# Kernel tuning notes

Measured on AMD Instinct MI355X. Metric: run time of the kernel, lower is better.

## Reference

```python
import jax, jax.numpy as jnp
import numpy as np

N = 65536   # nodes
D = 128     # in_dim == emb_dim (required by GRUCell usage)
E = 524288  # edges, pre-sorted by topological level
L = 8       # number of topological levels (edge_masks)


def _gru(x, h, Wi, Wh, bi, bh):
    # torch.nn.GRUCell semantics
    gi = x @ Wi.T + bi            # [*, 3D]
    gh = h @ Wh.T + bh
    ir, iz, i_n = jnp.split(gi, 3, axis=-1)
    hr, hz, h_n = jnp.split(gh, 3, axis=-1)
    r = jax.nn.sigmoid(ir + hr)
    z = jax.nn.sigmoid(iz + hz)
    n = jnp.tanh(i_n + r * h_n)
    return (1.0 - z) * n + z * h


def _direction(h_prev, j_lev, i_lev, ea_lev, We, be, Wa, ba, Wi, Wh, bi, bh):
    # j = message source (h_j gathered), i = aggregation target (segment index)
    n_nodes = h_prev.shape[0]
    # roots = nodes never appearing as aggregation target -> GRU with zero hidden
    root = ~jnp.zeros((n_nodes,), bool).at[i_lev.reshape(-1)].set(True)
    h = jnp.where(root[:, None], _gru(h_prev, jnp.zeros_like(h_prev), Wi, Wh, bi, bh), 0.0)

    def step(h, lev):
        j, i, ea = lev                       # [El], [El], [El, D]
        e = ea @ We.T + be                   # edge_lin
        q = h_prev[i]                        # h_prev_i
        k = h[j] + e                         # h_j + edge_emb
        v = h[j]
        alpha = (jnp.concatenate([q, k], axis=-1) @ Wa.T + ba)[:, 0]  # [El]
        # segment softmax over aggregation index i (numerically stable)
        m = jax.lax.stop_gradient(jax.ops.segment_max(alpha, i, num_segments=n_nodes))
        ex = jnp.exp(alpha - m[i])
        den = jax.ops.segment_sum(ex, i, num_segments=n_nodes)
        a = ex / den[i]
        msg = jax.ops.segment_sum(a[:, None] * v, i, num_segments=n_nodes)  # [N, D]
        mask = jnp.zeros((n_nodes,), bool).at[i].set(True)
        h_new = _gru(h_prev, msg, Wi, Wh, bi, bh)
        return jnp.where(mask[:, None], h_new, h), None

    h, _ = jax.lax.scan(step, h, (j_lev, i_lev, ea_lev))
    return h


def setup_inputs() -> dict:
    key = jax.random.key(0)
    ks = jax.random.split(key, 24)
    p = lambda k, shape: (0.05 * jax.random.normal(k, shape)).astype(jnp.float32)
    inp = {
        'x': jax.random.normal(ks[0], (N, D), jnp.float32),
        'edge_index': jax.random.randint(ks[1], (2, E), 0, N, dtype=jnp.int32),
        'edge_attr': jax.random.normal(ks[2], (E, D), jnp.float32),
        'num_levels': L,
        # forward-direction AttnConv + GRUCell params
        'We_f': p(ks[3], (D, D)), 'be_f': p(ks[4], (D,)),
        'Wa_f': p(ks[5], (1, 2 * D)), 'ba_f': p(ks[6], (1,)),
        'Wi_f': p(ks[7], (3 * D, D)), 'Wh_f': p(ks[8], (3 * D, D)),
        'bi_f': p(ks[9], (3 * D,)), 'bh_f': p(ks[10], (3 * D,)),
        # backward-direction params
        'We_b': p(ks[11], (D, D)), 'be_b': p(ks[12], (D,)),
        'Wa_b': p(ks[13], (1, 2 * D)), 'ba_b': p(ks[14], (1,)),
        'Wi_b': p(ks[15], (3 * D, D)), 'Wh_b': p(ks[16], (3 * D, D)),
        'bi_b': p(ks[17], (3 * D,)), 'bh_b': p(ks[18], (3 * D,)),
    }
    return inp


def reference(x, edge_index, edge_attr, num_levels,
              We_f, be_f, Wa_f, ba_f, Wi_f, Wh_f, bi_f, bh_f,
              We_b, be_b, Wa_b, ba_b, Wi_b, Wh_b, bi_b, bh_b):
    El = edge_index.shape[1] // num_levels
    src = edge_index[0].reshape(num_levels, El)
    dst = edge_index[1].reshape(num_levels, El)
    ea = edge_attr.reshape(num_levels, El, -1)
    # forward pass over levels: flow source->target, aggregate at dst
    h_fwd = _direction(x, src, dst, ea, We_f, be_f, Wa_f, ba_f, Wi_f, Wh_f, bi_f, bh_f)
    # fnb: backward pass takes h_fwd as h_prev; flow target->source (aggregate at src),
    # levels iterated in reverse
    h_bwd = _direction(h_fwd, dst[::-1], src[::-1], ea[::-1],
                       We_b, be_b, Wa_b, ba_b, Wi_b, Wh_b, bi_b, bh_b)
    return jax.nn.relu(h_bwd)
```

## Files before the change

kernel.cpp:

```cpp
#include <hip/hip_runtime.h>
#include <cstdint>
#include <cstddef>

constexpr int N_NODES = 65536;
constexpr int D       = 128;
constexpr int E_EDGES = 524288;
constexpr int LVLS    = 8;
constexpr int EL      = E_EDGES / LVLS;
constexpr int OSTR    = 65540;

typedef unsigned int  u32;
typedef unsigned short u16;
typedef __attribute__((ext_vector_type(8)))  short short8;
typedef __attribute__((ext_vector_type(16))) float f32x16;

__device__ __forceinline__ float sigmoidf_(float x) { return 1.0f / (1.0f + expf(-x)); }

__device__ __forceinline__ u32 bf_hi(float f) {
    u32 x = __float_as_uint(f);
    return (x + 0x7fffu + ((x >> 16) & 1u)) >> 16;
}
__device__ __forceinline__ float bf_f(u32 hbits) { return __uint_as_float(hbits << 16); }

__device__ __forceinline__ int swz(int row, int kbyte) {
    return row * 64 + (kbyte ^ ((row & 3) << 4));
}

__device__ __forceinline__ void gload_lds16(const void* g, void* l) {
    __builtin_amdgcn_global_load_lds(
        (const __attribute__((address_space(1))) unsigned int*)g,
        (__attribute__((address_space(3))) unsigned int*)l, 16, 0, 0);
}

__device__ __forceinline__ float wave_sum(float v) {
#pragma unroll
    for (int off = 32; off > 0; off >>= 1) v += __shfl_down(v, off, 64);
    return v;
}

__global__ __launch_bounds__(256)
void prep_kernel(const float* __restrict__ We_f, const float* __restrict__ Wa_f,
                 const float* __restrict__ be_f, const float* __restrict__ ba_f,
                 const float* __restrict__ We_b, const float* __restrict__ Wa_b,
                 const float* __restrict__ be_b, const float* __restrict__ ba_b,
                 float* __restrict__ u_f, float* __restrict__ u_b, float* __restrict__ cst)
{
    int t = threadIdx.x;
    if (t < 128) {
        float s = 0.f;
        for (int d = 0; d < 128; ++d) s = fmaf(We_f[d * 128 + t], Wa_f[128 + d], s);
        u_f[t] = s;
    } else {
        int c = t - 128;
        float s = 0.f;
        for (int d = 0; d < 128; ++d) s = fmaf(We_b[d * 128 + c], Wa_b[128 + d], s);
        u_b[c] = s;
    }
    if (t == 0) {
        float s = 0.f;
        for (int d = 0; d < 128; ++d) s = fmaf(be_f[d], Wa_f[128 + d], s);
        cst[0] = s + ba_f[0];
    }
    if (t == 255) {
        float s = 0.f;
        for (int d = 0; d < 128; ++d) s = fmaf(be_b[d], Wa_b[128 + d], s);
        cst[1] = s + ba_b[0];
    }
}

__global__ __launch_bounds__(256)
void convert_w(const float* __restrict__ W0, const float* __restrict__ W1,
               const float* __restrict__ W2, const float* __restrict__ W3,
               u16* __restrict__ hi4, u16* __restrict__ lo4)
{
    const float* Ws[4] = {W0, W1, W2, W3};
    int m = blockIdx.y;
    int i = blockIdx.x * 256 + threadIdx.x;
    int rw = i >> 7, k = i & 127;
    float v = Ws[m][i];
    u32 hb = bf_hi(v);
    hi4[(size_t)m * 49152 + i] = (u16)hb;
    if (rw >= 256)
        lo4[(size_t)m * 16384 + (size_t)(rw - 256) * 128 + k] = (u16)bf_hi(v - bf_f(hb));
}

__global__ __launch_bounds__(256)
void convert_x(const float* __restrict__ x, unsigned char* __restrict__ xhi,
               unsigned char* __restrict__ xlo)
{
    int idx = blockIdx.x * 256 + threadIdx.x;
    int n = idx >> 6, d = (idx & 63) << 1;
    float2 v = *reinterpret_cast<const float2*>(x + (size_t)n * 128 + d);
    u32 h0 = bf_hi(v.x), h1 = bf_hi(v.y);
    u32 l0 = bf_hi(v.x - bf_f(h0)), l1 = bf_hi(v.y - bf_f(h1));
    size_t off = (size_t)n * 256 + (size_t)d * 2;
    *reinterpret_cast<u32*>(xhi + off) = h0 | (h1 << 16);
    *reinterpret_cast<u32*>(xlo + off) = l0 | (l1 << 16);
}

__global__ __launch_bounds__(256)
void edot_kernel(const float* __restrict__ ea, const float* __restrict__ u_f,
                 const float* __restrict__ u_b, const float* __restrict__ cst,
                 float* __restrict__ edot_f, float* __restrict__ edot_b)
{
    int wv = threadIdx.x >> 6, lane = threadIdx.x & 63;
    int e = blockIdx.x * 4 + wv;
    if (e >= E_EDGES) return;
    int d = lane << 1;
    float2 v  = *reinterpret_cast<const float2*>(ea + (size_t)e * 128 + d);
    float2 uf = *reinterpret_cast<const float2*>(u_f + d);
    float2 ub = *reinterpret_cast<const float2*>(u_b + d);
    float af = wave_sum(v.x * uf.x + v.y * uf.y);
    float ab = wave_sum(v.x * ub.x + v.y * ub.y);
    if (lane == 0) {
        edot_f[e] = af + cst[0];
        edot_b[e] = ab + cst[1];
    }
}

__global__ __launch_bounds__(256)
void count_flags(const int* __restrict__ ei, int* __restrict__ counts,
                 int* __restrict__ flag_f, int* __restrict__ flag_b)
{
    int e = blockIdx.x * 256 + threadIdx.x;
    int lv = e >> 16;
    int s = ei[e], t = ei[E_EDGES + e];
    atomicAdd(&counts[(size_t)lv * 65536 + t], 1);
    atomicAdd(&counts[(size_t)(8 + lv) * 65536 + s], 1);
    flag_f[t] = 1;
    flag_b[s] = 1;
}

__global__ __launch_bounds__(1024)
void scan_compact(const int* __restrict__ counts, int* __restrict__ offs,
                  int* __restrict__ rows, int* __restrict__ cnts)
{
    __shared__ int sbuf[1024];
    __shared__ int nbuf[1024];
    int dl = blockIdx.x;
    const int4* c4 = reinterpret_cast<const int4*>(counts + (size_t)dl * 65536);
    int* o = offs + (size_t)dl * OSTR;
    int* rw = rows + (size_t)dl * 65536;
    int t = threadIdx.x;
    int cv[64];
#pragma unroll 4
    for (int k4 = 0; k4 < 16; ++k4) {
        int4 v = c4[t * 16 + k4];
        cv[k4 * 4 + 0] = v.x; cv[k4 * 4 + 1] = v.y;
        cv[k4 * 4 + 2] = v.z; cv[k4 * 4 + 3] = v.w;
    }
    int s = 0, nz = 0;
#pragma unroll
    for (int k = 0; k < 64; ++k) { s += cv[k]; nz += (cv[k] > 0); }
    sbuf[t] = s;
    nbuf[t] = nz;
    __syncthreads();
    int val = s, nval = nz;
    for (int off = 1; off < 1024; off <<= 1) {
        int add  = (t >= off) ? sbuf[t - off] : 0;
        int nadd = (t >= off) ? nbuf[t - off] : 0;
        __syncthreads();
        val += add;
        nval += nadd;
        sbuf[t] = val;
        nbuf[t] = nval;
        __syncthreads();
    }
    int run  = val - s;
    int nrun = nval - nz;
    int base = t * 64;
    int4* o4 = reinterpret_cast<int4*>(o + base);
#pragma unroll 4
    for (int k4 = 0; k4 < 16; ++k4) {
        int4 ov;
        ov.x = run; run += cv[k4 * 4 + 0];
        ov.y = run; run += cv[k4 * 4 + 1];
        ov.z = run; run += cv[k4 * 4 + 2];
        ov.w = run; run += cv[k4 * 4 + 3];
        o4[k4] = ov;
#pragma unroll
        for (int q = 0; q < 4; ++q)
            if (cv[k4 * 4 + q] > 0) rw[nrun++] = base + k4 * 4 + q;
    }
    if (t == 1023) { o[65536] = val; cnts[dl] = nval; }
}

__global__ __launch_bounds__(256)
void fill_csr(const int* __restrict__ ei, const float* __restrict__ edot_f,
              const float* __restrict__ edot_b, const int* __restrict__ offs,
              int* __restrict__ cursor, int2* __restrict__ csr)
{
    int idx = blockIdx.x * 256 + threadIdx.x;
    int dir = idx >= E_EDGES;
    int ge = dir ? idx - E_EDGES : idx;
    int lv = ge >> 16;
    int dl = dir * 8 + lv;
    int i = dir ? ei[ge] : ei[E_EDGES + ge];
    int j = dir ? ei[E_EDGES + ge] : ei[ge];
    int pos = offs[(size_t)dl * OSTR + i] + atomicAdd(&cursor[(size_t)dl * 65536 + i], 1);
    int2 v;
    v.x = j;
    v.y = __float_as_int(dir ? edot_b[ge] : edot_f[ge]);
    csr[(size_t)dl * EL + pos] = v;
}

__global__ __launch_bounds__(256)
void root_init(const float* __restrict__ hp, const int* __restrict__ flag,
               const float* __restrict__ Wi, const float* __restrict__ bi,
               const float* __restrict__ bh, const float* __restrict__ wa,
               float* __restrict__ h, unsigned char* __restrict__ h_hi,
               unsigned char* __restrict__ h_lo,
               float* __restrict__ qdot, float* __restrict__ hdot)
{
    int wv = threadIdx.x >> 6, lane = threadIdx.x & 63;
    int n = blockIdx.x * 4 + wv;
    int d = lane << 1;
    const float* hprow = hp + (size_t)n * 128;
    float2 hpv = *reinterpret_cast<const float2*>(hprow + d);
    float qd = wave_sum(hpv.x * wa[d] + hpv.y * wa[d + 1]);
    if (lane == 0) qdot[n] = qd;
    bool root = (flag[n] == 0);
    float hv[2] = {0.f, 0.f};
    if (root) {
#pragma unroll
        for (int q = 0; q < 2; ++q) {
            int dd = d + q;
            float g0 = bi[dd], g1 = bi[dd + 128], g2 = bi[dd + 256];
            for (int k = 0; k < 128; ++k) {
                float a = hprow[k];
                g0 = fmaf(a, Wi[(size_t)dd * 128 + k], g0);
                g1 = fmaf(a, Wi[(size_t)(dd + 128) * 128 + k], g1);
                g2 = fmaf(a, Wi[(size_t)(dd + 256) * 128 + k], g2);
            }
            float rr = sigmoidf_(g0 + bh[dd]);
            float zz = sigmoidf_(g1 + bh[dd + 128]);
            float nn = tanhf(g2 + rr * bh[dd + 256]);
            hv[q] = (1.f - zz) * nn;
        }
        *reinterpret_cast<float2*>(h + (size_t)n * 128 + d) = make_float2(hv[0], hv[1]);
        u32 hb0 = bf_hi(hv[0]), hb1 = bf_hi(hv[1]);
        u32 lb0 = bf_hi(hv[0] - bf_f(hb0)), lb1 = bf_hi(hv[1] - bf_f(hb1));
        size_t off = (size_t)n * 256 + (size_t)d * 2;
        *reinterpret_cast<u32*>(h_hi + off) = hb0 | (hb1 << 16);
        *reinterpret_cast<u32*>(h_lo + off) = lb0 | (lb1 << 16);
    }
    float hd = wave_sum(hv[0] * wa[128 + d] + hv[1] * wa[128 + d + 1]);
    if (lane == 0) hdot[n] = root ? hd : 0.f;
}

__global__ __launch_bounds__(256)
void attn_msg(const int* __restrict__ pcnt, const int* __restrict__ rows,
              const int* __restrict__ offs, const int2* __restrict__ csr,
              const float* __restrict__ qdot, const float* __restrict__ hdot,
              const float* __restrict__ h, unsigned char* __restrict__ msg_hi,
              unsigned char* __restrict__ msg_lo)
{
    int cnt = *pcnt;
    int l31 = threadIdx.x & 31;
    int hid = (blockIdx.x * 256 + threadIdx.x) >> 5;
    int nh = (gridDim.x * 256) >> 5;
    int d4 = l31 << 2;
    for (int r = hid; r < cnt; r += nh) {
        int i = rows[r];
        int o0 = offs[i], o1 = offs[i + 1];
        float qi = qdot[i];
        float den = 0.f;
        float4 acc = make_float4(0.f, 0.f, 0.f, 0.f);
        for (int e = o0; e < o1; ++e) {
            int2 je = csr[e];
            float ex = expf(qi + hdot[je.x] + __int_as_float(je.y));
            float4 hv = *reinterpret_cast<const float4*>(h + (size_t)je.x * 128 + d4);
            den += ex;
            acc.x = fmaf(ex, hv.x, acc.x);
            acc.y = fmaf(ex, hv.y, acc.y);
            acc.z = fmaf(ex, hv.z, acc.z);
            acc.w = fmaf(ex, hv.w, acc.w);
        }
        float inv = 1.f / den;
        float m0 = acc.x * inv, m1 = acc.y * inv, m2 = acc.z * inv, m3 = acc.w * inv;
        u32 h0 = bf_hi(m0), h1 = bf_hi(m1), h2 = bf_hi(m2), h3 = bf_hi(m3);
        u32 l0 = bf_hi(m0 - bf_f(h0)), l1 = bf_hi(m1 - bf_f(h1));
        u32 l2 = bf_hi(m2 - bf_f(h2)), l3 = bf_hi(m3 - bf_f(h3));
        size_t off = (size_t)r * 256 + (size_t)d4 * 2;
        *reinterpret_cast<uint2*>(msg_hi + off) = make_uint2(h0 | (h1 << 16), h2 | (h3 << 16));
        *reinterpret_cast<uint2*>(msg_lo + off) = make_uint2(l0 | (l1 << 16), l2 | (l3 << 16));
    }
}

__global__ __launch_bounds__(512, 1)
void gemm_gru(const unsigned char* __restrict__ msg_hi, const unsigned char* __restrict__ msg_lo,
              const unsigned char* __restrict__ hp_hi, const unsigned char* __restrict__ hp_lo,
              const u16* __restrict__ Whhi, const u16* __restrict__ Whlo,
              const u16* __restrict__ Wihi, const u16* __restrict__ Wilo,
              const int* __restrict__ pcnt, const int* __restrict__ rows,
              const float* __restrict__ bi, const float* __restrict__ bh,
              const float* __restrict__ wa,
              float* __restrict__ h, unsigned char* __restrict__ h_hi,
              unsigned char* __restrict__ h_lo, float* __restrict__ hdot)
{
    __shared__ __align__(16) unsigned char smem[32768 + 65536 + 2048 + 512];
    unsigned char* As = smem;
    unsigned char* Bs = smem + 32768;
    float* red   = (float*)(smem + 98304);
    int* rowsLds = (int*)(smem + 98304 + 2048);

    const int tid = threadIdx.x;
    const int cnt = *pcnt;
    const int row0 = blockIdx.x * 128;
    if (row0 >= cnt) return;

    if (tid < 128) {
        int gr = row0 + tid;
        rowsLds[tid] = (gr < cnt) ? rows[gr] : 0;
    }
    __syncthreads();

    const int lane = tid & 63, wv = tid >> 6;
    const int q = wv & 3, mh = wv >> 2;
    const int l31 = lane & 31, l5 = lane >> 5;

    const int rwA = wv * 16 + (lane >> 2);
    const int slA = ((lane & 3) << 4) ^ ((rwA & 3) << 4);
    const size_t baseA0 = (size_t)(row0 + rwA) * 256 + slA;
    const size_t baseA1 = (size_t)rowsLds[rwA] * 256 + slA;
    size_t bsrc[3];
#pragma unroll
    for (int k = 0; k < 3; ++k) {
        int rwB = wv * 48 + k * 16 + (lane >> 2);
        bsrc[k] = (size_t)rwB * 256 + (((lane & 3) << 4) ^ ((rwB & 3) << 4));
    }
    const int rwL = wv * 16 + (lane >> 2);
    const size_t lsrc = (size_t)rwL * 256 + (((lane & 3) << 4) ^ ((rwL & 3) << 4));

    f32x16 acc[2][3];
#pragma unroll
    for (int mt = 0; mt < 2; ++mt)
#pragma unroll
        for (int g = 0; g < 3; ++g) acc[mt][g] = (f32x16)0.0f;
    f32x16 ghn[2];

    auto STAGE = [&](int t, int b) {
        int ph = t >> 2, ks = t & 3;
        size_t ko = (size_t)ks * 64;
        const unsigned char* Ahi = ph ? hp_hi : msg_hi;
        const unsigned char* Alo = ph ? hp_lo : msg_lo;
        size_t ab = (ph ? baseA1 : baseA0) + ko;
        unsigned char* Ad = As + b * 16384 + wv * 1024;
        gload_lds16(Ahi + ab, Ad);
        gload_lds16(Alo + ab, Ad + 8192);
        const unsigned char* Bh = (const unsigned char*)(ph ? Wihi : Whhi);
        const unsigned char* Bl = (const unsigned char*)(ph ? Wilo : Whlo);
        unsigned char* Bd = Bs + b * 32768;
#pragma unroll
        for (int k = 0; k < 3; ++k)
            gload_lds16(Bh + bsrc[k] + ko, Bd + (wv * 3 + k) * 1024);
        gload_lds16(Bl + lsrc + ko, Bd + 24576 + wv * 1024);
    };

    STAGE(0, 0);
    for (int t = 0; t < 8; ++t) {
        int b = t & 1;
        if (t < 7) STAGE(t + 1, b ^ 1);
        __builtin_amdgcn_sched_barrier(0);
        if (t < 7) asm volatile("s_waitcnt vmcnt(6)");
        else       asm volatile("s_waitcnt vmcnt(0)");
        __builtin_amdgcn_s_barrier();
        __builtin_amdgcn_sched_barrier(0);

        const unsigned char* Ab = As + b * 16384;
        const unsigned char* Bb = Bs + b * 32768;
#pragma unroll
        for (int kh = 0; kh < 2; ++kh) {
            short8 a[2][2];
#pragma unroll
            for (int mt = 0; mt < 2; ++mt)
#pragma unroll
                for (int hf = 0; hf < 2; ++hf)
                    a[mt][hf] = *reinterpret_cast<const short8*>(
                        Ab + hf * 8192 + swz(mh * 64 + mt * 32 + l31, kh * 32 + l5 * 16));
            short8 b0 = *reinterpret_cast<const short8*>(
                Bb + swz(q * 32 + l31, kh * 32 + l5 * 16));
            short8 b1 = *reinterpret_cast<const short8*>(
                Bb + swz(q * 32 + 128 + l31, kh * 32 + l5 * 16));
            short8 b2 = *reinterpret_cast<const short8*>(
                Bb + swz(q * 32 + 256 + l31, kh * 32 + l5 * 16));
            short8 bl2 = *reinterpret_cast<const short8*>(
                Bb + 24576 + swz(q * 32 + l31, kh * 32 + l5 * 16));
#pragma unroll
            for (int mt = 0; mt < 2; ++mt) {
                acc[mt][0] = __builtin_amdgcn_mfma_f32_32x32x16_bf16(a[mt][0], b0, acc[mt][0], 0, 0, 0);
                acc[mt][0] = __builtin_amdgcn_mfma_f32_32x32x16_bf16(a[mt][1], b0, acc[mt][0], 0, 0, 0);
                acc[mt][1] = __builtin_amdgcn_mfma_f32_32x32x16_bf16(a[mt][0], b1, acc[mt][1], 0, 0, 0);
                acc[mt][1] = __builtin_amdgcn_mfma_f32_32x32x16_bf16(a[mt][1], b1, acc[mt][1], 0, 0, 0);
                acc[mt][2] = __builtin_amdgcn_mfma_f32_32x32x16_bf16(a[mt][0], b2, acc[mt][2], 0, 0, 0);
                acc[mt][2] = __builtin_amdgcn_mfma_f32_32x32x16_bf16(a[mt][0], bl2, acc[mt][2], 0, 0, 0);
                acc[mt][2] = __builtin_amdgcn_mfma_f32_32x32x16_bf16(a[mt][1], b2, acc[mt][2], 0, 0, 0);
            }
        }
        if (t == 3) {
            ghn[0] = acc[0][2];
            ghn[1] = acc[1][2];
            acc[0][2] = (f32x16)0.0f;
            acc[1][2] = (f32x16)0.0f;
        }
        __builtin_amdgcn_s_barrier();
        __builtin_amdgcn_sched_barrier(0);
    }

    const int d = q * 32 + l31;
    const float wa2d = wa[128 + d];
    const float bi0 = bi[d], bi1 = bi[d + 128], bi2 = bi[d + 256];
    const float bh0 = bh[d], bh1 = bh[d + 128], bh2 = bh[d + 256];

#pragma unroll
    for (int mt = 0; mt < 2; ++mt)
#pragma unroll
        for (int rg = 0; rg < 16; ++rg) {
            int rl = mh * 64 + mt * 32 + (rg & 3) + ((rg >> 2) << 3) + (l5 << 2);
            int gr = row0 + rl;
            bool ok = gr < cnt;
            int n = rowsLds[rl];
            u16 mhb = *reinterpret_cast<const u16*>(msg_hi + (size_t)gr * 256 + (size_t)d * 2);
            u16 mlb = *reinterpret_cast<const u16*>(msg_lo + (size_t)gr * 256 + (size_t)d * 2);
            float mval = bf_f(mhb) + bf_f(mlb);
            float rr = sigmoidf_(acc[mt][0][rg] + bi0 + bh0);
            float zz = sigmoidf_(acc[mt][1][rg] + bi1 + bh1);
            float nn = tanhf(acc[mt][2][rg] + bi2 + rr * (ghn[mt][rg] + bh2));
            float hv = (1.f - zz) * nn + zz * mval;
            if (ok) {
                h[(size_t)n * 128 + d] = hv;
                u32 hb = bf_hi(hv);
                *reinterpret_cast<u16*>(h_hi + (size_t)n * 256 + (size_t)d * 2) = (u16)hb;
                *reinterpret_cast<u16*>(h_lo + (size_t)n * 256 + (size_t)d * 2) =
                    (u16)bf_hi(hv - bf_f(hb));
            }
            float pd = hv * wa2d;
#pragma unroll
            for (int o = 1; o < 32; o <<= 1) pd += __shfl_xor(pd, o, 64);
            if (l31 == 0) red[rl * 4 + q] = pd;
        }
    __syncthreads();
    if (tid < 128 && row0 + tid < cnt) {
        int n = rowsLds[tid];
        hdot[n] = red[tid * 4] + red[tid * 4 + 1] + red[tid * 4 + 2] + red[tid * 4 + 3];
    }
}

__global__ __launch_bounds__(256)
void relu_kernel(const float* __restrict__ h, float* __restrict__ out)
{
    int idx = (blockIdx.x * 256 + threadIdx.x) * 4;
    float4 v = *reinterpret_cast<const float4*>(h + idx);
    v.x = fmaxf(v.x, 0.f); v.y = fmaxf(v.y, 0.f);
    v.z = fmaxf(v.z, 0.f); v.w = fmaxf(v.w, 0.f);
    *reinterpret_cast<float4*>(out + idx) = v;
}

extern "C" void kernel_launch(void* const* d_in, const int* in_sizes, int n_in,
                              void* d_out, int out_size, void* d_ws, size_t ws_size,
                              hipStream_t stream)
{
    (void)in_sizes; (void)n_in; (void)out_size; (void)ws_size;

    const float* x    = (const float*)d_in[0];
    const int*   ei   = (const int*)d_in[1];
    const float* ea   = (const float*)d_in[2];
    const float* We_f = (const float*)d_in[4];
    const float* be_f = (const float*)d_in[5];
    const float* Wa_f = (const float*)d_in[6];
    const float* ba_f = (const float*)d_in[7];
    const float* Wi_f = (const float*)d_in[8];
    const float* Wh_f = (const float*)d_in[9];
    const float* bi_f = (const float*)d_in[10];
    const float* bh_f = (const float*)d_in[11];
    const float* We_b = (const float*)d_in[12];
    const float* be_b = (const float*)d_in[13];
    const float* Wa_b = (const float*)d_in[14];
    const float* ba_b = (const float*)d_in[15];
    const float* Wi_b = (const float*)d_in[16];
    const float* Wh_b = (const float*)d_in[17];
    const float* bi_b = (const float*)d_in[18];
    const float* bh_b = (const float*)d_in[19];
    float* out = (float*)d_out;

    char* p = (char*)d_ws;
    auto carve = [&](size_t bytes) -> char* {
        char* r = p;
        p += (bytes + 255) & ~(size_t)255;
        return r;
    };
    int*   counts  = (int*)carve((size_t)16 * 65536 * 4);
    int*   cursor  = (int*)carve((size_t)16 * 65536 * 4);
    int*   flag_f  = (int*)carve((size_t)N_NODES * 4);
    int*   flag_b  = (int*)carve((size_t)N_NODES * 4);
    float* h_fwd   = (float*)carve((size_t)N_NODES * D * 4);
    float* h_cur   = (float*)carve((size_t)N_NODES * D * 4);
    unsigned char* hf_hi = (unsigned char*)carve((size_t)N_NODES * 256);
    unsigned char* hf_lo = (unsigned char*)carve((size_t)N_NODES * 256);
    size_t zbytes  = (size_t)((char*)hf_lo - (char*)counts) + (size_t)N_NODES * 256;
    int*   cnts    = (int*)carve(256);
    u16*   Whi4    = (u16*)carve((size_t)4 * 49152 * 2);
    u16*   Wlo4    = (u16*)carve((size_t)4 * 16384 * 2);
    unsigned char* x_hi  = (unsigned char*)carve((size_t)N_NODES * 256);
    unsigned char* x_lo  = (unsigned char*)carve((size_t)N_NODES * 256);
    unsigned char* hc_hi = (unsigned char*)carve((size_t)N_NODES * 256);
    unsigned char* hc_lo = (unsigned char*)carve((size_t)N_NODES * 256);
    unsigned char* msg_hi= (unsigned char*)carve((size_t)N_NODES * 256);
    unsigned char* msg_lo= (unsigned char*)carve((size_t)N_NODES * 256);
    float* u_f     = (float*)carve((size_t)D * 4);
    float* u_b     = (float*)carve((size_t)D * 4);
    float* cst     = (float*)carve(16);
    float* edot_f  = (float*)carve((size_t)E_EDGES * 4);
    float* edot_b  = (float*)carve((size_t)E_EDGES * 4);
    int*   offs    = (int*)carve((size_t)16 * OSTR * 4);
    int2*  csr     = (int2*)carve((size_t)16 * EL * 8);
    int*   rows    = (int*)carve((size_t)16 * 65536 * 4);
    float* qdot    = (float*)carve((size_t)N_NODES * 4);
    float* hdot    = (float*)carve((size_t)N_NODES * 4);

    hipMemsetAsync(counts, 0, zbytes, stream);
    prep_kernel<<<1, 256, 0, stream>>>(We_f, Wa_f, be_f, ba_f, We_b, Wa_b, be_b, ba_b,
                                       u_f, u_b, cst);
    convert_w<<<dim3(192, 4), 256, 0, stream>>>(Wi_f, Wh_f, Wi_b, Wh_b, Whi4, Wlo4);
    convert_x<<<16384, 256, 0, stream>>>(x, x_hi, x_lo);
    count_flags<<<E_EDGES / 256, 256, 0, stream>>>(ei, counts, flag_f, flag_b);
    edot_kernel<<<E_EDGES / 4, 256, 0, stream>>>(ea, u_f, u_b, cst, edot_f, edot_b);
    scan_compact<<<16, 1024, 0, stream>>>(counts, offs, rows, cnts);
    fill_csr<<<2 * E_EDGES / 256, 256, 0, stream>>>(ei, edot_f, edot_b, offs, cursor, csr);

    for (int dir = 0; dir < 2; ++dir) {
        const float* hp   = dir == 0 ? x : h_fwd;
        float*       h    = dir == 0 ? h_fwd : h_cur;
        const unsigned char* hp_hi = dir == 0 ? x_hi : hf_hi;
        const unsigned char* hp_lo = dir == 0 ? x_lo : hf_lo;
        unsigned char* h_hi = dir == 0 ? hf_hi : hc_hi;
        unsigned char* h_lo = dir == 0 ? hf_lo : hc_lo;
        const u16* Wihi = Whi4 + (size_t)(dir * 2) * 49152;
        const u16* Whhi = Whi4 + (size_t)(dir * 2 + 1) * 49152;
        const u16* Wilo = Wlo4 + (size_t)(dir * 2) * 16384;
        const u16* Whlo = Wlo4 + (size_t)(dir * 2 + 1) * 16384;
        const float* Wi   = dir == 0 ? Wi_f : Wi_b;
        const float* bi   = dir == 0 ? bi_f : bi_b;
        const float* bh   = dir == 0 ? bh_f : bh_b;
        const float* wa   = dir == 0 ? Wa_f : Wa_b;
        const int*   flag = dir == 0 ? flag_f : flag_b;

        root_init<<<N_NODES / 4, 256, 0, stream>>>(hp, flag, Wi, bi, bh, wa,
                                                   h, h_hi, h_lo, qdot, hdot);

        for (int t = 0; t < LVLS; ++t) {
            int lv = dir == 0 ? t : (LVLS - 1 - t);
            int dl = dir * LVLS + lv;
            attn_msg<<<2048, 256, 0, stream>>>(
                cnts + dl, rows + (size_t)dl * 65536, offs + (size_t)dl * OSTR,
                csr + (size_t)dl * EL, qdot, hdot, h, msg_hi, msg_lo);
            gemm_gru<<<512, 512, 0, stream>>>(
                msg_hi, msg_lo, hp_hi, hp_lo, Whhi, Whlo, Wihi, Wilo,
                cnts + dl, rows + (size_t)dl * 65536,
                bi, bh, wa, h, h_hi, h_lo, hdot);
        }
    }
    relu_kernel<<<(N_NODES * D) / 1024, 256, 0, stream>>>(h_cur, out);
}
```

Before: 1.702 ms.

## Fuse attention message aggregation into GRU GEMM kernel via LDS-resident messages

Merges the attention/segment-softmax message kernel into the GEMM+GRU kernel, so each block computes its 128 rows' messages directly into shared memory as bf16 hi/lo tiles instead of round-tripping them through global memory. Because h is read by gathers while being updated, results go to a staging buffer and a separate commit kernel scatters them back into h and hdot. The backward direction also stops writing bf16 images of h it never reads. In exchange, LDS use doubles, which limits occupancy, and the gather-bound message phase now runs inside a one-block-per-CU kernel, with an extra commit launch per level.

```diff
diff --git a/kernel.cpp b/kernel.cpp
--- a/kernel.cpp
+++ b/kernel.cpp
@@ -209,7 +209,7 @@
                const float* __restrict__ Wi, const float* __restrict__ bi,
                const float* __restrict__ bh, const float* __restrict__ wa,
                float* __restrict__ h, unsigned char* __restrict__ h_hi,
-               unsigned char* __restrict__ h_lo,
+               unsigned char* __restrict__ h_lo, int write_img,
                float* __restrict__ qdot, float* __restrict__ hdot)
 {
     int wv = threadIdx.x >> 6, lane = threadIdx.x & 63;
@@ -238,91 +238,52 @@
             hv[q] = (1.f - zz) * nn;
         }
         *reinterpret_cast<float2*>(h + (size_t)n * 128 + d) = make_float2(hv[0], hv[1]);
-        u32 hb0 = bf_hi(hv[0]), hb1 = bf_hi(hv[1]);
-        u32 lb0 = bf_hi(hv[0] - bf_f(hb0)), lb1 = bf_hi(hv[1] - bf_f(hb1));
-        size_t off = (size_t)n * 256 + (size_t)d * 2;
-        *reinterpret_cast<u32*>(h_hi + off) = hb0 | (hb1 << 16);
-        *reinterpret_cast<u32*>(h_lo + off) = lb0 | (lb1 << 16);
+        if (write_img) {
+            u32 hb0 = bf_hi(hv[0]), hb1 = bf_hi(hv[1]);
+            u32 lb0 = bf_hi(hv[0] - bf_f(hb0)), lb1 = bf_hi(hv[1] - bf_f(hb1));
+            size_t off = (size_t)n * 256 + (size_t)d * 2;
+            *reinterpret_cast<u32*>(h_hi + off) = hb0 | (hb1 << 16);
+            *reinterpret_cast<u32*>(h_lo + off) = lb0 | (lb1 << 16);
+        }
     }
     float hd = wave_sum(hv[0] * wa[128 + d] + hv[1] * wa[128 + d + 1]);
     if (lane == 0) hdot[n] = root ? hd : 0.f;
 }
 
-__global__ __launch_bounds__(256)
-void attn_msg(const int* __restrict__ pcnt, const int* __restrict__ rows,
-              const int* __restrict__ offs, const int2* __restrict__ csr,
-              const float* __restrict__ qdot, const float* __restrict__ hdot,
-              const float* __restrict__ h, unsigned char* __restrict__ msg_hi,
-              unsigned char* __restrict__ msg_lo)
-{
-    int cnt = *pcnt;
-    int l31 = threadIdx.x & 31;
-    int hid = (blockIdx.x * 256 + threadIdx.x) >> 5;
-    int nh = (gridDim.x * 256) >> 5;
-    int d4 = l31 << 2;
-    for (int r = hid; r < cnt; r += nh) {
-        int i = rows[r];
-        int o0 = offs[i], o1 = offs[i + 1];
-        float qi = qdot[i];
-        float den = 0.f;
-        float4 acc = make_float4(0.f, 0.f, 0.f, 0.f);
-        for (int e = o0; e < o1; ++e) {
-            int2 je = csr[e];
-            float ex = expf(qi + hdot[je.x] + __int_as_float(je.y));
-            float4 hv = *reinterpret_cast<const float4*>(h + (size_t)je.x * 128 + d4);
-            den += ex;
-            acc.x = fmaf(ex, hv.x, acc.x);
-            acc.y = fmaf(ex, hv.y, acc.y);
-            acc.z = fmaf(ex, hv.z, acc.z);
-            acc.w = fmaf(ex, hv.w, acc.w);
-        }
-        float inv = 1.f / den;
-        float m0 = acc.x * inv, m1 = acc.y * inv, m2 = acc.z * inv, m3 = acc.w * inv;
-        u32 h0 = bf_hi(m0), h1 = bf_hi(m1), h2 = bf_hi(m2), h3 = bf_hi(m3);
-        u32 l0 = bf_hi(m0 - bf_f(h0)), l1 = bf_hi(m1 - bf_f(h1));
-        u32 l2 = bf_hi(m2 - bf_f(h2)), l3 = bf_hi(m3 - bf_f(h3));
-        size_t off = (size_t)r * 256 + (size_t)d4 * 2;
-        *reinterpret_cast<uint2*>(msg_hi + off) = make_uint2(h0 | (h1 << 16), h2 | (h3 << 16));
-        *reinterpret_cast<uint2*>(msg_lo + off) = make_uint2(l0 | (l1 << 16), l2 | (l3 << 16));
-    }
-}
-
 __global__ __launch_bounds__(512, 1)
-void gemm_gru(const unsigned char* __restrict__ msg_hi, const unsigned char* __restrict__ msg_lo,
-              const unsigned char* __restrict__ hp_hi, const unsigned char* __restrict__ hp_lo,
-              const u16* __restrict__ Whhi, const u16* __restrict__ Whlo,
-              const u16* __restrict__ Wihi, const u16* __restrict__ Wilo,
-              const int* __restrict__ pcnt, const int* __restrict__ rows,
-              const float* __restrict__ bi, const float* __restrict__ bh,
-              const float* __restrict__ wa,
-              float* __restrict__ h, unsigned char* __restrict__ h_hi,
-              unsigned char* __restrict__ h_lo, float* __restrict__ hdot)
-{
-    __shared__ __align__(16) unsigned char smem[32768 + 65536 + 2048 + 512];
+void level_kernel(const int* __restrict__ pcnt, const int* __restrict__ rows,
+                  const int* __restrict__ offs, const int2* __restrict__ csr,
+                  const float* __restrict__ qdot, const float* __restrict__ hdot,
+                  const float* __restrict__ hsrc,
+                  const unsigned char* __restrict__ hp_hi, const unsigned char* __restrict__ hp_lo,
+                  const u16* __restrict__ Whhi, const u16* __restrict__ Whlo,
+                  const u16* __restrict__ Wihi, const u16* __restrict__ Wilo,
+                  const float* __restrict__ bi, const float* __restrict__ bh,
+                  const float* __restrict__ wa,
+                  float* __restrict__ h_stage, float* __restrict__ hdot_stage,
+                  unsigned char* __restrict__ h_hi, unsigned char* __restrict__ h_lo,
+                  int write_img)
+{
+    __shared__ __align__(16) unsigned char smem[65536 + 65536 + 2048 + 512];
     unsigned char* As = smem;
-    unsigned char* Bs = smem + 32768;
-    float* red   = (float*)(smem + 98304);
-    int* rowsLds = (int*)(smem + 98304 + 2048);
+    unsigned char* Bs = smem + 65536;
+    float* red   = (float*)(smem + 131072);
+    int* rowsLds = (int*)(smem + 131072 + 2048);
 
     const int tid = threadIdx.x;
     const int cnt = *pcnt;
     const int row0 = blockIdx.x * 128;
     if (row0 >= cnt) return;
 
+    const int lane = tid & 63, wv = tid >> 6;
+    const int q = wv & 3, mh = wv >> 2;
+    const int l31 = lane & 31, l5 = lane >> 5;
+
     if (tid < 128) {
         int gr = row0 + tid;
         rowsLds[tid] = (gr < cnt) ? rows[gr] : 0;
     }
-    __syncthreads();
-
-    const int lane = tid & 63, wv = tid >> 6;
-    const int q = wv & 3, mh = wv >> 2;
-    const int l31 = lane & 31, l5 = lane >> 5;
-
-    const int rwA = wv * 16 + (lane >> 2);
-    const int slA = ((lane & 3) << 4) ^ ((rwA & 3) << 4);
-    const size_t baseA0 = (size_t)(row0 + rwA) * 256 + slA;
-    const size_t baseA1 = (size_t)rowsLds[rwA] * 256 + slA;
+
     size_t bsrc[3];
 #pragma unroll
     for (int k = 0; k < 3; ++k) {
@@ -331,6 +292,68 @@
     }
     const int rwL = wv * 16 + (lane >> 2);
     const size_t lsrc = (size_t)rwL * 256 + (((lane & 3) << 4) ^ ((rwL & 3) << 4));
+    const int rwA = wv * 16 + (lane >> 2);
+    const int slA = ((lane & 3) << 4) ^ ((rwA & 3) << 4);
+
+    {
+        unsigned char* Bd = Bs;
+#pragma unroll
+        for (int k = 0; k < 3; ++k)
+            gload_lds16((const unsigned char*)Whhi + bsrc[k], Bd + (wv * 3 + k) * 1024);
+        gload_lds16((const unsigned char*)Whlo + lsrc, Bd + 24576 + wv * 1024);
+    }
+
+    __syncthreads();
+    const size_t baseA1 = (size_t)rowsLds[rwA] * 256 + slA;
+
+    {
+        int hw = tid >> 5;
+        int d0 = l31 << 2;
+        int ks = l31 >> 3;
+        int kb = (l31 & 7) << 3;
+        for (int k = 0; k < 8; ++k) {
+            int rl = hw + 16 * k;
+            int i = rowsLds[rl];
+            int o0 = offs[i], o1 = offs[i + 1];
+            float qi = qdot[i];
+            float den = 0.f;
+            float4 acc4 = make_float4(0.f, 0.f, 0.f, 0.f);
+            for (int e = o0; e < o1; ++e) {
+                int2 je = csr[e];
+                float ex = expf(qi + hdot[je.x] + __int_as_float(je.y));
+                float4 hv = *reinterpret_cast<const float4*>(hsrc + (size_t)je.x * 128 + d0);
+                den += ex;
+                acc4.x = fmaf(ex, hv.x, acc4.x);
+                acc4.y = fmaf(ex, hv.y, acc4.y);
+                acc4.z = fmaf(ex, hv.z, acc4.z);
+                acc4.w = fmaf(ex, hv.w, acc4.w);
+            }
+            float inv = 1.f / den;
+            float m0 = acc4.x * inv, m1 = acc4.y * inv;
+            float m2 = acc4.z * inv, m3 = acc4.w * inv;
+            u32 h0 = bf_hi(m0), h1 = bf_hi(m1), h2 = bf_hi(m2), h3 = bf_hi(m3);
+            u32 l0 = bf_hi(m0 - bf_f(h0)), l1 = bf_hi(m1 - bf_f(h1));
+            u32 l2 = bf_hi(m2 - bf_f(h2)), l3 = bf_hi(m3 - bf_f(h3));
+            int off = ks * 8192 + swz(rl, kb);
+            *reinterpret_cast<uint2*>(As + off)         = make_uint2(h0 | (h1 << 16), h2 | (h3 << 16));
+            *reinterpret_cast<uint2*>(As + 32768 + off) = make_uint2(l0 | (l1 << 16), l2 | (l3 << 16));
+        }
+    }
+    __syncthreads();
+
+    float mval[2][16];
+#pragma unroll
+    for (int mt = 0; mt < 2; ++mt)
+#pragma unroll
+        for (int rg = 0; rg < 16; ++rg) {
+            int rl = mh * 64 + mt * 32 + (rg & 3) + ((rg >> 2) << 3) + (l5 << 2);
+            int off = q * 8192 + swz(rl, l31 * 2);
+            u16 hb = *reinterpret_cast<const u16*>(As + off);
+            u16 lb = *reinterpret_cast<const u16*>(As + 32768 + off);
+            mval[mt][rg] = bf_f(hb) + bf_f(lb);
+        }
+    asm volatile("s_waitcnt lgkmcnt(0)");
+    __builtin_amdgcn_sched_barrier(0);
 
     f32x16 acc[2][3];
 #pragma unroll
@@ -339,45 +362,50 @@
         for (int g = 0; g < 3; ++g) acc[mt][g] = (f32x16)0.0f;
     f32x16 ghn[2];
 
-    auto STAGE = [&](int t, int b) {
-        int ph = t >> 2, ks = t & 3;
-        size_t ko = (size_t)ks * 64;
-        const unsigned char* Ahi = ph ? hp_hi : msg_hi;
-        const unsigned char* Alo = ph ? hp_lo : msg_lo;
-        size_t ab = (ph ? baseA1 : baseA0) + ko;
-        unsigned char* Ad = As + b * 16384 + wv * 1024;
-        gload_lds16(Ahi + ab, Ad);
-        gload_lds16(Alo + ab, Ad + 8192);
-        const unsigned char* Bh = (const unsigned char*)(ph ? Wihi : Whhi);
-        const unsigned char* Bl = (const unsigned char*)(ph ? Wilo : Whlo);
+    auto STAGE = [&](int tt) {
+        int b = tt & 1;
         unsigned char* Bd = Bs + b * 32768;
-#pragma unroll
-        for (int k = 0; k < 3; ++k)
-            gload_lds16(Bh + bsrc[k] + ko, Bd + (wv * 3 + k) * 1024);
-        gload_lds16(Bl + lsrc + ko, Bd + 24576 + wv * 1024);
+        if (tt >= 4) {
+            size_t ko = (size_t)(tt - 4) * 64;
+            unsigned char* Ad = As + b * 16384 + wv * 1024;
+            gload_lds16(hp_hi + baseA1 + ko, Ad);
+            gload_lds16(hp_lo + baseA1 + ko, Ad + 8192);
+#pragma unroll
+            for (int k = 0; k < 3; ++k)
+                gload_lds16((const unsigned char*)Wihi + bsrc[k] + ko, Bd + (wv * 3 + k) * 1024);
+            gload_lds16((const unsigned char*)Wilo + lsrc + ko, Bd + 24576 + wv * 1024);
+        } else {
+            size_t ko = (size_t)tt * 64;
+#pragma unroll
+            for (int k = 0; k < 3; ++k)
+                gload_lds16((const unsigned char*)Whhi + bsrc[k] + ko, Bd + (wv * 3 + k) * 1024);
+            gload_lds16((const unsigned char*)Whlo + lsrc + ko, Bd + 24576 + wv * 1024);
+        }
     };
 
-    STAGE(0, 0);
     for (int t = 0; t < 8; ++t) {
-        int b = t & 1;
-        if (t < 7) STAGE(t + 1, b ^ 1);
+        if (t < 7) STAGE(t + 1);
         __builtin_amdgcn_sched_barrier(0);
-        if (t < 7) asm volatile("s_waitcnt vmcnt(6)");
-        else       asm volatile("s_waitcnt vmcnt(0)");
+        if (t < 3)      asm volatile("s_waitcnt vmcnt(4)");
+        else if (t < 7) asm volatile("s_waitcnt vmcnt(6)");
+        else            asm volatile("s_waitcnt vmcnt(0)");
         __builtin_amdgcn_s_barrier();
         __builtin_amdgcn_sched_barrier(0);
 
-        const unsigned char* Ab = As + b * 16384;
-        const unsigned char* Bb = Bs + b * 32768;
+        const unsigned char *a_hi, *a_lo;
+        if (t < 4) { a_hi = As + t * 8192;          a_lo = As + 32768 + t * 8192; }
+        else       { a_hi = As + (t & 1) * 16384;   a_lo = a_hi + 8192; }
+        const unsigned char* Bb = Bs + (t & 1) * 32768;
 #pragma unroll
         for (int kh = 0; kh < 2; ++kh) {
             short8 a[2][2];
 #pragma unroll
-            for (int mt = 0; mt < 2; ++mt)
-#pragma unroll
-                for (int hf = 0; hf < 2; ++hf)
-                    a[mt][hf] = *reinterpret_cast<const short8*>(
-                        Ab + hf * 8192 + swz(mh * 64 + mt * 32 + l31, kh * 32 + l5 * 16));
+            for (int mt = 0; mt < 2; ++mt) {
+                a[mt][0] = *reinterpret_cast<const short8*>(
+                    a_hi + swz(mh * 64 + mt * 32 + l31, kh * 32 + l5 * 16));
+                a[mt][1] = *reinterpret_cast<const short8*>(
+                    a_lo + swz(mh * 64 + mt * 32 + l31, kh * 32 + l5 * 16));
+            }
             short8 b0 = *reinterpret_cast<const short8*>(
                 Bb + swz(q * 32 + l31, kh * 32 + l5 * 16));
             short8 b1 = *reinterpret_cast<const short8*>(
@@ -420,19 +448,18 @@
             int gr = row0 + rl;
             bool ok = gr < cnt;
             int n = rowsLds[rl];
-            u16 mhb = *reinterpret_cast<const u16*>(msg_hi + (size_t)gr * 256 + (size_t)d * 2);
-            u16 mlb = *reinterpret_cast<const u16*>(msg_lo + (size_t)gr * 256 + (size_t)d * 2);
-            float mval = bf_f(mhb) + bf_f(mlb);
             float rr = sigmoidf_(acc[mt][0][rg] + bi0 + bh0);
             float zz = sigmoidf_(acc[mt][1][rg] + bi1 + bh1);
             float nn = tanhf(acc[mt][2][rg] + bi2 + rr * (ghn[mt][rg] + bh2));
-            float hv = (1.f - zz) * nn + zz * mval;
+            float hv = (1.f - zz) * nn + zz * mval[mt][rg];
             if (ok) {
-                h[(size_t)n * 128 + d] = hv;
-                u32 hb = bf_hi(hv);
-                *reinterpret_cast<u16*>(h_hi + (size_t)n * 256 + (size_t)d * 2) = (u16)hb;
-                *reinterpret_cast<u16*>(h_lo + (size_t)n * 256 + (size_t)d * 2) =
-                    (u16)bf_hi(hv - bf_f(hb));
+                h_stage[(size_t)gr * 128 + d] = hv;
+                if (write_img) {
+                    u32 hb = bf_hi(hv);
+                    *reinterpret_cast<u16*>(h_hi + (size_t)n * 256 + (size_t)d * 2) = (u16)hb;
+                    *reinterpret_cast<u16*>(h_lo + (size_t)n * 256 + (size_t)d * 2) =
+                        (u16)bf_hi(hv - bf_f(hb));
+                }
             }
             float pd = hv * wa2d;
 #pragma unroll
@@ -440,9 +467,26 @@
             if (l31 == 0) red[rl * 4 + q] = pd;
         }
     __syncthreads();
-    if (tid < 128 && row0 + tid < cnt) {
-        int n = rowsLds[tid];
-        hdot[n] = red[tid * 4] + red[tid * 4 + 1] + red[tid * 4 + 2] + red[tid * 4 + 3];
+    if (tid < 128 && row0 + tid < cnt)
+        hdot_stage[row0 + tid] = red[tid * 4] + red[tid * 4 + 1] +
+                                 red[tid * 4 + 2] + red[tid * 4 + 3];
+}
+
+__global__ __launch_bounds__(256)
+void commit_kernel(const int* __restrict__ pcnt, const int* __restrict__ rows,
+                   const float* __restrict__ h_stage, const float* __restrict__ hdot_stage,
+                   float* __restrict__ h, float* __restrict__ hdot)
+{
+    int cnt = *pcnt;
+    int wv = threadIdx.x >> 6, lane = threadIdx.x & 63;
+    int r0 = blockIdx.x * 4 + wv;
+    int nw = gridDim.x * 4;
+    int d = lane << 1;
+    for (int r = r0; r < cnt; r += nw) {
+        int n = rows[r];
+        float2 v = *reinterpret_cast<const float2*>(h_stage + (size_t)r * 128 + d);
+        *reinterpret_cast<float2*>(h + (size_t)n * 128 + d) = v;
+        if (lane == 0) hdot[n] = hdot_stage[r];
     }
 }
 
@@ -495,18 +539,16 @@
     int*   flag_b  = (int*)carve((size_t)N_NODES * 4);
     float* h_fwd   = (float*)carve((size_t)N_NODES * D * 4);
     float* h_cur   = (float*)carve((size_t)N_NODES * D * 4);
+    size_t zbytes  = (size_t)((char*)h_cur - (char*)counts) + (size_t)N_NODES * D * 4;
     unsigned char* hf_hi = (unsigned char*)carve((size_t)N_NODES * 256);
     unsigned char* hf_lo = (unsigned char*)carve((size_t)N_NODES * 256);
-    size_t zbytes  = (size_t)((char*)hf_lo - (char*)counts) + (size_t)N_NODES * 256;
     int*   cnts    = (int*)carve(256);
     u16*   Whi4    = (u16*)carve((size_t)4 * 49152 * 2);
     u16*   Wlo4    = (u16*)carve((size_t)4 * 16384 * 2);
     unsigned char* x_hi  = (unsigned char*)carve((size_t)N_NODES * 256);
     unsigned char* x_lo  = (unsigned char*)carve((size_t)N_NODES * 256);
-    unsigned char* hc_hi = (unsigned char*)carve((size_t)N_NODES * 256);
-    unsigned char* hc_lo = (unsigned char*)carve((size_t)N_NODES * 256);
-    unsigned char* msg_hi= (unsigned char*)carve((size_t)N_NODES * 256);
-    unsigned char* msg_lo= (unsigned char*)carve((size_t)N_NODES * 256);
+    float* h_stage = (float*)carve((size_t)N_NODES * D * 4);
+    float* hdot_stage = (float*)carve((size_t)N_NODES * 4);
     float* u_f     = (float*)carve((size_t)D * 4);
     float* u_b     = (float*)carve((size_t)D * 4);
     float* cst     = (float*)carve(16);
@@ -533,8 +575,9 @@
         float*       h    = dir == 0 ? h_fwd : h_cur;
         const unsigned char* hp_hi = dir == 0 ? x_hi : hf_hi;
         const unsigned char* hp_lo = dir == 0 ? x_lo : hf_lo;
-        unsigned char* h_hi = dir == 0 ? hf_hi : hc_hi;
-        unsigned char* h_lo = dir == 0 ? hf_lo : hc_lo;
+        unsigned char* h_hi = hf_hi;
+        unsigned char* h_lo = hf_lo;
+        int write_img = (dir == 0);
         const u16* Wihi = Whi4 + (size_t)(dir * 2) * 49152;
         const u16* Whhi = Whi4 + (size_t)(dir * 2 + 1) * 49152;
         const u16* Wilo = Wlo4 + (size_t)(dir * 2) * 16384;
@@ -546,18 +589,18 @@
         const int*   flag = dir == 0 ? flag_f : flag_b;
 
         root_init<<<N_NODES / 4, 256, 0, stream>>>(hp, flag, Wi, bi, bh, wa,
-                                                   h, h_hi, h_lo, qdot, hdot);
+                                                   h, h_hi, h_lo, write_img, qdot, hdot);
 
         for (int t = 0; t < LVLS; ++t) {
             int lv = dir == 0 ? t : (LVLS - 1 - t);
             int dl = dir * LVLS + lv;
-            attn_msg<<<2048, 256, 0, stream>>>(
+            level_kernel<<<512, 512, 0, stream>>>(
                 cnts + dl, rows + (size_t)dl * 65536, offs + (size_t)dl * OSTR,
-                csr + (size_t)dl * EL, qdot, hdot, h, msg_hi, msg_lo);
-            gemm_gru<<<512, 512, 0, stream>>>(
-                msg_hi, msg_lo, hp_hi, hp_lo, Whhi, Whlo, Wihi, Wilo,
-                cnts + dl, rows + (size_t)dl * 65536,
-                bi, bh, wa, h, h_hi, h_lo, hdot);
+                csr + (size_t)dl * EL, qdot, hdot, h,
+                hp_hi, hp_lo, Whhi, Whlo, Wihi, Wilo,
+                bi, bh, wa, h_stage, hdot_stage, h_hi, h_lo, write_img);
+            commit_kernel<<<1024, 256, 0, stream>>>(
+                cnts + dl, rows + (size_t)dl * 65536, h_stage, hdot_stage, h, hdot);
         }
     }
     relu_kernel<<<(N_NODES * D) / 1024, 256, 0, stream>>>(h_cur, out);
```

Result: slower. 2.154 ms (+26.6%).
